# Performance work log

Hardware: AMD Instinct MI355X
Metric: run time of the kernel (lower is better)

## Reference

```python
import jax, jax.numpy as jnp
import numpy as np

N, T, D, H = 32, 4096, 256, 512  # n_mlps, tokens per mlp, d_model, hidden


def setup_inputs() -> dict:
    key = jax.random.key(0)
    k_x, k_w1, k_w2 = jax.random.split(key, 3)
    x = jax.random.normal(k_x, (N, T, D), dtype=jnp.float32)
    # per-MLP weights stacked along the expert dim; init ~ torch Linear default scale
    W1 = jax.random.normal(k_w1, (N, H, D), dtype=jnp.float32) / np.sqrt(D)
    b1 = jnp.zeros((N, H), dtype=jnp.float32)
    W2 = jax.random.normal(k_w2, (N, D, H), dtype=jnp.float32) / np.sqrt(H)
    b2 = jnp.zeros((N, D), dtype=jnp.float32)
    return {"x": x, "W1": W1, "b1": b1, "W2": W2, "b2": b2}


def reference(x, W1, b1, W2, b2):
    # outputs[i] = mlp_i(x[i]); stack + residual add.
    # Expressed as a single grouped (batched) GEMM over the expert dim n.
    h = jnp.einsum('ntd,nhd->nth', x, W1) + b1[:, None, :]   # [N,T,H]
    h = jax.nn.silu(h)
    out = jnp.einsum('nth,ndh->ntd', h, W2) + b2[:, None, :]  # [N,T,D]
    return out + x
```

## Files before the change

### kernel.cpp

```cpp
#include <hip/hip_runtime.h>
#include <hip/hip_bf16.h>


#define N_EXP 32
#define T_TOK 4096
#define D_MOD 256
#define H_HID 512

#define BT 64
#define HC 32
#define NCHUNK 16
#define NTHREADS 256

#define NWELEM 4194304ull
#define WS_NEEDED (8ull * NWELEM)

typedef __attribute__((ext_vector_type(8))) __bf16 bf16x8;
typedef __attribute__((ext_vector_type(4))) __bf16 bf16x4;
typedef __attribute__((ext_vector_type(4))) float  f32x4;
union U4 { uint4 q; bf16x8 v; };

static __device__ __forceinline__ f32x4 mfma16(bf16x8 a, bf16x8 b, f32x4 c) {
  return __builtin_amdgcn_mfma_f32_16x16x32_bf16(a, b, c, 0, 0, 0);
}

static __device__ __forceinline__ void split8(const float v[8], bf16x8& hi, bf16x8& lo) {
#pragma unroll
  for (int j = 0; j < 8; ++j) {
    float f = v[j];
    __bf16 h = (__bf16)f;
    hi[j] = h;
    lo[j] = (__bf16)(f - (float)h);
  }
}

static __device__ __forceinline__ void gl_lds16(const __bf16* g, __bf16* l) {
  __builtin_amdgcn_global_load_lds(
      (const __attribute__((address_space(1))) void*)g,
      (__attribute__((address_space(3))) void*)l, 16, 0, 0);
}

#define BAR_LGKM() do { asm volatile("s_waitcnt lgkmcnt(0)" ::: "memory"); \
  __builtin_amdgcn_s_barrier(); __builtin_amdgcn_sched_barrier(0); } while (0)
#define BAR_VM(n) do { asm volatile("s_waitcnt vmcnt(" #n ")" ::: "memory"); \
  __builtin_amdgcn_s_barrier(); __builtin_amdgcn_sched_barrier(0); } while (0)

__global__ __launch_bounds__(256)
void presplit_w(const float* __restrict__ W1, const float* __restrict__ W2,
                __bf16* __restrict__ ws) {
  unsigned U = blockIdx.x * 256 + threadIdx.x;
  {
    unsigned row = U >> 5;
    unsigned u   = U & 31;
    const float* src = W1 + ((size_t)U << 3);
    float4 a0 = *(const float4*)src, a1 = *(const float4*)(src + 4);
    float v[8] = {a0.x, a0.y, a0.z, a0.w, a1.x, a1.y, a1.z, a1.w};
    bf16x8 hi, lo; split8(v, hi, lo);
    size_t dst = (((size_t)row << 5) | (u ^ (row & 7))) << 3;
    *(bf16x8*)(ws + dst)          = hi;
    *(bf16x8*)(ws + NWELEM + dst) = lo;
  }
  {
    unsigned r = U >> 6;
    unsigned e = r >> 8, d = r & 255;
    unsigned u = U & 63;
    unsigned c = u >> 2, uc = u & 3;
    const float* src = W2 + ((size_t)U << 3);
    float4 a0 = *(const float4*)src, a1 = *(const float4*)(src + 4);
    float v[8] = {a0.x, a0.y, a0.z, a0.w, a1.x, a1.y, a1.z, a1.w};
    bf16x8 hi, lo; split8(v, hi, lo);
    size_t dst = (((((size_t)((e << 4) + c) << 8) + d) << 2) | (uc ^ ((d >> 1) & 3))) << 3;
    *(bf16x8*)(ws + 2 * NWELEM + dst) = hi;
    *(bf16x8*)(ws + 3 * NWELEM + dst) = lo;
  }
}

__global__ __launch_bounds__(NTHREADS, 2)
void pmlp_fused(const float* __restrict__ x, const float* __restrict__ b1g,
                const float* __restrict__ b2g, float* __restrict__ out,
                const __bf16* __restrict__ wsp) {
  __shared__ __bf16 W1h[HC * D_MOD],   W1l[HC * D_MOD];
  __shared__ __bf16 W2h[D_MOD * HC],   W2l[D_MOD * HC];
  __shared__ unsigned APK[BT * 32];
  __shared__ float b1s[H_HID];

  const int tid = threadIdx.x;

  const int p    = blockIdx.x;
  const int xcd  = p & 7;
  const int slot = p >> 3;
  const int e    = xcd + ((slot >> 6) << 3);
  const int ti   = slot & 63;

  const float* xb = x + ((size_t)e * T_TOK + (size_t)ti * BT) * D_MOD;
  float*       ob = out + ((size_t)e * T_TOK + (size_t)ti * BT) * D_MOD;

  const int l    = tid & 63;
  const int w    = tid >> 6;
  const int lrow = l & 15;
  const int lk8  = (l >> 4) << 3;
  const int lr4  = (l >> 4) << 2;
  const int g1_r = w << 4;

  b1s[tid]       = b1g[e * H_HID + tid];
  b1s[tid + 256] = b1g[e * H_HID + tid + 256];

  bf16x8 xh[8], xl[8];
#pragma unroll
  for (int kk = 0; kk < 8; ++kk) {
    const float* s = xb + (g1_r + lrow) * D_MOD + (kk << 5) + lk8;
    float4 u0 = *(const float4*)s;
    float4 u1 = *(const float4*)(s + 4);
    float v[8] = {u0.x, u0.y, u0.z, u0.w, u1.x, u1.y, u1.z, u1.w};
    split8(v, xh[kk], xl[kk]);
  }

  const __bf16* w1h_img = wsp;
  const __bf16* w1l_img = wsp + NWELEM;
  const __bf16* w2h_img = wsp + 2 * NWELEM;
  const __bf16* w2l_img = wsp + 3 * NWELEM;

  auto stageW1 = [&](int c) {
    size_t gb = ((size_t)(e * NCHUNK + c)) << 13;
#pragma unroll
    for (int s = 0; s < 4; ++s) {
      int off = ((w << 2) + s) << 9;
      int go  = off + (l << 3);
      gl_lds16(w1h_img + gb + go, &W1h[off]);
      gl_lds16(w1l_img + gb + go, &W1l[off]);
    }
  };
  auto stageW2 = [&](int c) {
    size_t gb = ((size_t)(e * NCHUNK + c)) << 13;
#pragma unroll
    for (int s = 0; s < 4; ++s) {
      int off = ((w << 2) + s) << 9;
      int go  = off + (l << 3);
      gl_lds16(w2h_img + gb + go, &W2h[off]);
      gl_lds16(w2l_img + gb + go, &W2l[off]);
    }
  };

  const f32x4 fz = {0.f, 0.f, 0.f, 0.f};
  f32x4 acc2[4][4];
#pragma unroll
  for (int mf = 0; mf < 4; ++mf)
#pragma unroll
    for (int nf = 0; nf < 4; ++nf) acc2[mf][nf] = fz;

  asm volatile("" ::: "memory");
  stageW1(0);
  stageW2(0);
  asm volatile("s_waitcnt vmcnt(8)\n\ts_waitcnt lgkmcnt(0)" ::: "memory");
  __builtin_amdgcn_s_barrier();
  __builtin_amdgcn_sched_barrier(0);

  for (int c = 0; c < NCHUNK; ++c) {
    f32x4 acc1[2] = {fz, fz};
    __builtin_amdgcn_s_setprio(1);
#pragma unroll
    for (int kk = 0; kk < 8; ++kk) {
#pragma unroll
      for (int cf = 0; cf < 2; ++cf) {
        int r1 = (cf << 4) + lrow;
        int uu = (((kk << 2) + (lk8 >> 3)) ^ (r1 & 7)) << 3;
        bf16x8 bh = *(const bf16x8*)&W1h[(r1 << 8) + uu];
        bf16x8 bl = *(const bf16x8*)&W1l[(r1 << 8) + uu];
        acc1[cf] = mfma16(xh[kk], bh, acc1[cf]);
        acc1[cf] = mfma16(xh[kk], bl, acc1[cf]);
        acc1[cf] = mfma16(xl[kk], bh, acc1[cf]);
      }
    }
    __builtin_amdgcn_s_setprio(0);
#pragma unroll
    for (int cf = 0; cf < 2; ++cf) {
      int acol = (cf << 4) + lrow;
      float b1v = b1s[c * HC + acol];
#pragma unroll
      for (int r = 0; r < 4; ++r) {
        float hv = acc1[cf][r] + b1v;
        hv = hv / (1.f + __expf(-hv));
        __bf16 hh = (__bf16)hv;
        __bf16 hl = (__bf16)(hv - (float)hh);
        unsigned pk = (unsigned)__builtin_bit_cast(unsigned short, hh) |
                      ((unsigned)__builtin_bit_cast(unsigned short, hl) << 16);
        int arow = g1_r + lr4 + r;
        APK[arow * 32 + ((((acol >> 2) ^ (arow & 7)) << 2) | (acol & 3))] = pk;
      }
    }
    BAR_LGKM();

    if (c < NCHUNK - 1) {
      stageW1(c + 1);
      BAR_VM(8);
    } else {
      BAR_VM(0);
    }

    bf16x8 bh2[4], bl2[4];
#pragma unroll
    for (int nf = 0; nf < 4; ++nf) {
      int dcol = (w << 6) + (nf << 4) + lrow;
      int up = (((lk8 >> 3) ^ ((dcol >> 1) & 3)) << 3);
      bh2[nf] = *(const bf16x8*)&W2h[(dcol << 5) + up];
      bl2[nf] = *(const bf16x8*)&W2l[(dcol << 5) + up];
    }
#pragma unroll
    for (int mf = 0; mf < 4; ++mf) {
      int m  = (mf << 4) + lrow;
      int u1 = lk8 >> 2;
      uint4 qa = *(const uint4*)&APK[m * 32 + ((u1 ^ (m & 7)) << 2)];
      uint4 qb = *(const uint4*)&APK[m * 32 + (((u1 + 1) ^ (m & 7)) << 2)];
      U4 ah, al;
      ah.q.x = (qa.x & 0xFFFFu) | (qa.y << 16);
      ah.q.y = (qa.z & 0xFFFFu) | (qa.w << 16);
      ah.q.z = (qb.x & 0xFFFFu) | (qb.y << 16);
      ah.q.w = (qb.z & 0xFFFFu) | (qb.w << 16);
      al.q.x = (qa.x >> 16) | (qa.y & 0xFFFF0000u);
      al.q.y = (qa.z >> 16) | (qa.w & 0xFFFF0000u);
      al.q.z = (qb.x >> 16) | (qb.y & 0xFFFF0000u);
      al.q.w = (qb.z >> 16) | (qb.w & 0xFFFF0000u);
      __builtin_amdgcn_s_setprio(1);
#pragma unroll
      for (int nf = 0; nf < 4; ++nf) {
        acc2[mf][nf] = mfma16(ah.v, bh2[nf], acc2[mf][nf]);
        acc2[mf][nf] = mfma16(ah.v, bl2[nf], acc2[mf][nf]);
        acc2[mf][nf] = mfma16(al.v, bh2[nf], acc2[mf][nf]);
      }
      __builtin_amdgcn_s_setprio(0);
    }
    BAR_LGKM();

    if (c < NCHUNK - 1) {
      stageW2(c + 1);
      BAR_VM(8);
    }
  }

#pragma unroll
  for (int mf = 0; mf < 4; ++mf)
#pragma unroll
    for (int r = 0; r < 4; ++r) {
      int trow = (mf << 4) + lr4 + r;
#pragma unroll
      for (int nf = 0; nf < 4; ++nf) {
        int dcol = (w << 6) + (nf << 4) + lrow;
        ob[trow * D_MOD + dcol] = acc2[mf][nf][r] + b2g[e * D_MOD + dcol]
                                + xb[trow * D_MOD + dcol];
      }
    }
}

#define WPITCH 264
__global__ __launch_bounds__(NTHREADS, 2)
void pmlp_fb(const float* __restrict__ x, const float* __restrict__ W1,
             const float* __restrict__ b1, const float* __restrict__ W2,
             const float* __restrict__ b2, float* __restrict__ out) {
  __shared__ __bf16 W1h[HC * WPITCH], W1l[HC * WPITCH];
  __shared__ __bf16 W2h[D_MOD * 32],  W2l[D_MOD * 32];
  __shared__ unsigned APK[BT * 32];

  const int tid = threadIdx.x;
  const int p = blockIdx.x, xcd = p & 7, slot = p >> 3;
  const int e = xcd + ((slot >> 6) << 3), ti = slot & 63;
  const float* xb = x + ((size_t)e * T_TOK + (size_t)ti * BT) * D_MOD;
  float*       ob = out + ((size_t)e * T_TOK + (size_t)ti * BT) * D_MOD;
  const int l = tid & 63, w = tid >> 6;
  const int lrow = l & 15, lk8 = (l >> 4) << 3, lr4 = (l >> 4) << 2;
  const int g1_r = w << 4;

  bf16x8 xh[8], xl[8];
#pragma unroll
  for (int kk = 0; kk < 8; ++kk) {
    const float* s = xb + (g1_r + lrow) * D_MOD + (kk << 5) + lk8;
    float4 u0 = *(const float4*)s, u1 = *(const float4*)(s + 4);
    float v[8] = {u0.x, u0.y, u0.z, u0.w, u1.x, u1.y, u1.z, u1.w};
    split8(v, xh[kk], xl[kk]);
  }

  float s1[4][8], s2[4][8];
  auto loadW = [&](int c) {
#pragma unroll
    for (int k2 = 0; k2 < 4; ++k2) {
      int g = tid + (k2 << 8);
      int r1 = g >> 5, c1 = (g & 31) << 3;
      int r2 = g >> 2, c2 = (g & 3) << 3;
      const float* sp1 = W1 + ((size_t)e * H_HID + c * HC + r1) * D_MOD + c1;
      const float* sp2 = W2 + ((size_t)e * D_MOD + r2) * H_HID + c * HC + c2;
      float4 u0 = *(const float4*)sp1, u1 = *(const float4*)(sp1 + 4);
      s1[k2][0]=u0.x; s1[k2][1]=u0.y; s1[k2][2]=u0.z; s1[k2][3]=u0.w;
      s1[k2][4]=u1.x; s1[k2][5]=u1.y; s1[k2][6]=u1.z; s1[k2][7]=u1.w;
      float4 v0 = *(const float4*)sp2, v1 = *(const float4*)(sp2 + 4);
      s2[k2][0]=v0.x; s2[k2][1]=v0.y; s2[k2][2]=v0.z; s2[k2][3]=v0.w;
      s2[k2][4]=v1.x; s2[k2][5]=v1.y; s2[k2][6]=v1.z; s2[k2][7]=v1.w;
    }
  };
  auto writeW = [&]() {
#pragma unroll
    for (int k2 = 0; k2 < 4; ++k2) {
      int g = tid + (k2 << 8);
      int r1 = g >> 5, c1 = (g & 31) << 3;
      int r2 = g >> 2, u2 = g & 3;
      int sw2 = ((u2 ^ (r2 & 3)) << 3);
      bf16x8 hi, lo;
      split8(s1[k2], hi, lo);
      *(bf16x8*)&W1h[r1 * WPITCH + c1] = hi;
      *(bf16x8*)&W1l[r1 * WPITCH + c1] = lo;
      split8(s2[k2], hi, lo);
      *(bf16x8*)&W2h[r2 * 32 + sw2] = hi;
      *(bf16x8*)&W2l[r2 * 32 + sw2] = lo;
    }
  };

  const f32x4 fz = {0.f, 0.f, 0.f, 0.f};
  f32x4 acc2[4][4];
#pragma unroll
  for (int mf = 0; mf < 4; ++mf)
#pragma unroll
    for (int nf = 0; nf < 4; ++nf) acc2[mf][nf] = fz;

  loadW(0); writeW();
  __syncthreads();

  for (int c = 0; c < NCHUNK; ++c) {
    if (c < NCHUNK - 1) loadW(c + 1);
    f32x4 acc1[2] = {fz, fz};
#pragma unroll
    for (int kk = 0; kk < 8; ++kk) {
#pragma unroll
      for (int cf = 0; cf < 2; ++cf) {
        int r1 = (cf << 4) + lrow;
        int k = (kk << 5) + lk8;
        bf16x8 bh = *(const bf16x8*)&W1h[r1 * WPITCH + k];
        bf16x8 bl = *(const bf16x8*)&W1l[r1 * WPITCH + k];
        acc1[cf] = mfma16(xh[kk], bh, acc1[cf]);
        acc1[cf] = mfma16(xh[kk], bl, acc1[cf]);
        acc1[cf] = mfma16(xl[kk], bh, acc1[cf]);
      }
    }
#pragma unroll
    for (int cf = 0; cf < 2; ++cf) {
      int acol = (cf << 4) + lrow;
      float b1v = b1[e * H_HID + c * HC + acol];
#pragma unroll
      for (int r = 0; r < 4; ++r) {
        float hv = acc1[cf][r] + b1v;
        hv = hv / (1.f + __expf(-hv));
        __bf16 hh = (__bf16)hv;
        __bf16 hl = (__bf16)(hv - (float)hh);
        unsigned pk = (unsigned)__builtin_bit_cast(unsigned short, hh) |
                      ((unsigned)__builtin_bit_cast(unsigned short, hl) << 16);
        int arow = g1_r + lr4 + r;
        APK[arow * 32 + ((((acol >> 2) ^ (arow & 7)) << 2) | (acol & 3))] = pk;
      }
    }
    __syncthreads();

    bf16x8 bh2[4], bl2[4];
#pragma unroll
    for (int nf = 0; nf < 4; ++nf) {
      int dcol = (w << 6) + (nf << 4) + lrow;
      int sw = (((lk8 >> 3) ^ (dcol & 3)) << 3);
      bh2[nf] = *(const bf16x8*)&W2h[dcol * 32 + sw];
      bl2[nf] = *(const bf16x8*)&W2l[dcol * 32 + sw];
    }
#pragma unroll
    for (int mf = 0; mf < 4; ++mf) {
      int m = (mf << 4) + lrow, u1 = lk8 >> 2;
      uint4 qa = *(const uint4*)&APK[m * 32 + ((u1 ^ (m & 7)) << 2)];
      uint4 qb = *(const uint4*)&APK[m * 32 + (((u1 + 1) ^ (m & 7)) << 2)];
      U4 ah, al;
      ah.q.x = (qa.x & 0xFFFFu) | (qa.y << 16);
      ah.q.y = (qa.z & 0xFFFFu) | (qa.w << 16);
      ah.q.z = (qb.x & 0xFFFFu) | (qb.y << 16);
      ah.q.w = (qb.z & 0xFFFFu) | (qb.w << 16);
      al.q.x = (qa.x >> 16) | (qa.y & 0xFFFF0000u);
      al.q.y = (qa.z >> 16) | (qa.w & 0xFFFF0000u);
      al.q.z = (qb.x >> 16) | (qb.y & 0xFFFF0000u);
      al.q.w = (qb.z >> 16) | (qb.w & 0xFFFF0000u);
#pragma unroll
      for (int nf = 0; nf < 4; ++nf) {
        acc2[mf][nf] = mfma16(ah.v, bh2[nf], acc2[mf][nf]);
        acc2[mf][nf] = mfma16(ah.v, bl2[nf], acc2[mf][nf]);
        acc2[mf][nf] = mfma16(al.v, bh2[nf], acc2[mf][nf]);
      }
    }
    __syncthreads();
    if (c < NCHUNK - 1) { writeW(); __syncthreads(); }
  }

#pragma unroll
  for (int mf = 0; mf < 4; ++mf)
#pragma unroll
    for (int r = 0; r < 4; ++r) {
      int trow = (mf << 4) + lr4 + r;
#pragma unroll
      for (int nf = 0; nf < 4; ++nf) {
        int dcol = (w << 6) + (nf << 4) + lrow;
        ob[trow * D_MOD + dcol] = acc2[mf][nf][r] + b2[e * D_MOD + dcol]
                                + xb[trow * D_MOD + dcol];
      }
    }
}

extern "C" void kernel_launch(void* const* d_in, const int* in_sizes, int n_in,
                              void* d_out, int out_size, void* d_ws, size_t ws_size,
                              hipStream_t stream) {
  const float* x  = (const float*)d_in[0];
  const float* W1 = (const float*)d_in[1];
  const float* b1 = (const float*)d_in[2];
  const float* W2 = (const float*)d_in[3];
  const float* b2 = (const float*)d_in[4];
  float* out = (float*)d_out;
  __bf16* ws = (__bf16*)d_ws;

  dim3 grid(N_EXP * (T_TOK / BT));
  dim3 block(NTHREADS);

  if (ws_size >= WS_NEEDED) {
    hipLaunchKernelGGL(presplit_w, dim3(2048), dim3(256), 0, stream, W1, W2, ws);
    hipLaunchKernelGGL(pmlp_fused, grid, block, 0, stream,
                       x, b1, b2, out, (const __bf16*)ws);
  } else {
    hipLaunchKernelGGL(pmlp_fb, grid, block, 0, stream, x, W1, b1, W2, b2, out);
  }
}
```

Before: 439.7 us.

## Load W2 fragments directly to registers and split activation LDS into hi/lo arrays

Re-lays out the presplit W2 image in MFMA fragment order so each wave loads its W2 B-operands straight from global memory into registers, dropping the W2 LDS staging and one barrier per chunk. The packed hi/lo activation buffer becomes two separate swizzled bf16 arrays, which removes the unpack bit-twiddling, and the first GEMM splits its accumulators into even and odd chains to shorten MFMA dependency chains. This frees LDS and cuts synchronisation, but the W2 register prefetch raises register pressure and relies on global-load latency being hidden behind the next chunk's first GEMM.

```diff
diff --git a/kernel.cpp b/kernel.cpp
--- a/kernel.cpp
+++ b/kernel.cpp
@@ -18,7 +18,6 @@
 typedef __attribute__((ext_vector_type(8))) __bf16 bf16x8;
 typedef __attribute__((ext_vector_type(4))) __bf16 bf16x4;
 typedef __attribute__((ext_vector_type(4))) float  f32x4;
-union U4 { uint4 q; bf16x8 v; };
 
 static __device__ __forceinline__ f32x4 mfma16(bf16x8 a, bf16x8 b, f32x4 c) {
   return __builtin_amdgcn_mfma_f32_16x16x32_bf16(a, b, c, 0, 0, 0);
@@ -42,7 +41,8 @@
 
 #define BAR_LGKM() do { asm volatile("s_waitcnt lgkmcnt(0)" ::: "memory"); \
   __builtin_amdgcn_s_barrier(); __builtin_amdgcn_sched_barrier(0); } while (0)
-#define BAR_VM(n) do { asm volatile("s_waitcnt vmcnt(" #n ")" ::: "memory"); \
+#define BAR_VM_LGKM(n) do { \
+  asm volatile("s_waitcnt vmcnt(" #n ") lgkmcnt(0)" ::: "memory"); \
   __builtin_amdgcn_s_barrier(); __builtin_amdgcn_sched_barrier(0); } while (0)
 
 __global__ __launch_bounds__(256)
@@ -61,17 +61,19 @@
     *(bf16x8*)(ws + NWELEM + dst) = lo;
   }
   {
-    unsigned r = U >> 6;
-    unsigned e = r >> 8, d = r & 255;
-    unsigned u = U & 63;
-    unsigned c = u >> 2, uc = u & 3;
+    unsigned uh = U & 63;
+    unsigned r  = U >> 6;
+    unsigned e  = r >> 8, d = r & 255;
+    unsigned c  = uh >> 2, kg = uh & 3;
+    unsigned w  = d >> 6, nf = (d >> 4) & 3;
+    unsigned lane = kg * 16 + (d & 15);
     const float* src = W2 + ((size_t)U << 3);
     float4 a0 = *(const float4*)src, a1 = *(const float4*)(src + 4);
     float v[8] = {a0.x, a0.y, a0.z, a0.w, a1.x, a1.y, a1.z, a1.w};
     bf16x8 hi, lo; split8(v, hi, lo);
-    size_t dst = (((((size_t)((e << 4) + c) << 8) + d) << 2) | (uc ^ ((d >> 1) & 3))) << 3;
-    *(bf16x8*)(ws + 2 * NWELEM + dst) = hi;
-    *(bf16x8*)(ws + 3 * NWELEM + dst) = lo;
+    size_t V = ((((size_t)(e * 16 + c) * 4 + w) * 4 + nf) * 64 + lane) << 3;
+    *(bf16x8*)(ws + 2 * NWELEM + V) = hi;
+    *(bf16x8*)(ws + 3 * NWELEM + V) = lo;
   }
 }
 
@@ -79,10 +81,9 @@
 void pmlp_fused(const float* __restrict__ x, const float* __restrict__ b1g,
                 const float* __restrict__ b2g, float* __restrict__ out,
                 const __bf16* __restrict__ wsp) {
-  __shared__ __bf16 W1h[HC * D_MOD],   W1l[HC * D_MOD];
-  __shared__ __bf16 W2h[D_MOD * HC],   W2l[D_MOD * HC];
-  __shared__ unsigned APK[BT * 32];
-  __shared__ float b1s[H_HID];
+  __shared__ __bf16 W1h[HC * D_MOD], W1l[HC * D_MOD];
+  __shared__ __bf16 Ah[BT * HC],     Al[BT * HC];
+  __shared__ float  b1s[H_HID];
 
   const int tid = threadIdx.x;
 
@@ -129,15 +130,17 @@
       gl_lds16(w1h_img + gb + go, &W1h[off]);
       gl_lds16(w1l_img + gb + go, &W1l[off]);
     }
+    __builtin_amdgcn_sched_barrier(0);
   };
-  auto stageW2 = [&](int c) {
-    size_t gb = ((size_t)(e * NCHUNK + c)) << 13;
-#pragma unroll
-    for (int s = 0; s < 4; ++s) {
-      int off = ((w << 2) + s) << 9;
-      int go  = off + (l << 3);
-      gl_lds16(w2h_img + gb + go, &W2h[off]);
-      gl_lds16(w2l_img + gb + go, &W2l[off]);
+
+  bf16x8 bh2[4], bl2[4];
+  auto loadW2 = [&](int c) {
+    size_t base = (((size_t)(e * NCHUNK + c) * 4 + w) * 4) << 9;
+#pragma unroll
+    for (int nf = 0; nf < 4; ++nf) {
+      size_t o = base + (((size_t)nf << 6) + l) * 8;
+      bh2[nf] = *(const bf16x8*)(w2h_img + o);
+      bl2[nf] = *(const bf16x8*)(w2l_img + o);
     }
   };
 
@@ -150,13 +153,13 @@
 
   asm volatile("" ::: "memory");
   stageW1(0);
-  stageW2(0);
-  asm volatile("s_waitcnt vmcnt(8)\n\ts_waitcnt lgkmcnt(0)" ::: "memory");
+  loadW2(0);
+  asm volatile("s_waitcnt vmcnt(8) lgkmcnt(0)" ::: "memory");
   __builtin_amdgcn_s_barrier();
   __builtin_amdgcn_sched_barrier(0);
 
   for (int c = 0; c < NCHUNK; ++c) {
-    f32x4 acc1[2] = {fz, fz};
+    f32x4 a1e[2] = {fz, fz}, a1o[2] = {fz, fz};
     __builtin_amdgcn_s_setprio(1);
 #pragma unroll
     for (int kk = 0; kk < 8; ++kk) {
@@ -166,74 +169,54 @@
         int uu = (((kk << 2) + (lk8 >> 3)) ^ (r1 & 7)) << 3;
         bf16x8 bh = *(const bf16x8*)&W1h[(r1 << 8) + uu];
         bf16x8 bl = *(const bf16x8*)&W1l[(r1 << 8) + uu];
-        acc1[cf] = mfma16(xh[kk], bh, acc1[cf]);
-        acc1[cf] = mfma16(xh[kk], bl, acc1[cf]);
-        acc1[cf] = mfma16(xl[kk], bh, acc1[cf]);
+        f32x4* acc = (kk & 1) ? &a1o[cf] : &a1e[cf];
+        *acc = mfma16(xh[kk], bh, *acc);
+        *acc = mfma16(xh[kk], bl, *acc);
+        *acc = mfma16(xl[kk], bh, *acc);
       }
     }
     __builtin_amdgcn_s_setprio(0);
+
 #pragma unroll
     for (int cf = 0; cf < 2; ++cf) {
       int acol = (cf << 4) + lrow;
       float b1v = b1s[c * HC + acol];
+      f32x4 hsum = a1e[cf] + a1o[cf];
 #pragma unroll
       for (int r = 0; r < 4; ++r) {
-        float hv = acc1[cf][r] + b1v;
+        float hv = hsum[r] + b1v;
         hv = hv / (1.f + __expf(-hv));
         __bf16 hh = (__bf16)hv;
         __bf16 hl = (__bf16)(hv - (float)hh);
-        unsigned pk = (unsigned)__builtin_bit_cast(unsigned short, hh) |
-                      ((unsigned)__builtin_bit_cast(unsigned short, hl) << 16);
         int arow = g1_r + lr4 + r;
-        APK[arow * 32 + ((((acol >> 2) ^ (arow & 7)) << 2) | (acol & 3))] = pk;
+        int idx = (arow << 5) + (((acol >> 3) ^ ((arow >> 1) & 3)) << 3) + (acol & 7);
+        Ah[idx] = hh;
+        Al[idx] = hl;
       }
     }
     BAR_LGKM();
 
-    if (c < NCHUNK - 1) {
-      stageW1(c + 1);
-      BAR_VM(8);
-    } else {
-      BAR_VM(0);
-    }
-
-    bf16x8 bh2[4], bl2[4];
-#pragma unroll
-    for (int nf = 0; nf < 4; ++nf) {
-      int dcol = (w << 6) + (nf << 4) + lrow;
-      int up = (((lk8 >> 3) ^ ((dcol >> 1) & 3)) << 3);
-      bh2[nf] = *(const bf16x8*)&W2h[(dcol << 5) + up];
-      bl2[nf] = *(const bf16x8*)&W2l[(dcol << 5) + up];
-    }
+    if (c < NCHUNK - 1) stageW1(c + 1);
+
 #pragma unroll
     for (int mf = 0; mf < 4; ++mf) {
       int m  = (mf << 4) + lrow;
-      int u1 = lk8 >> 2;
-      uint4 qa = *(const uint4*)&APK[m * 32 + ((u1 ^ (m & 7)) << 2)];
-      uint4 qb = *(const uint4*)&APK[m * 32 + (((u1 + 1) ^ (m & 7)) << 2)];
-      U4 ah, al;
-      ah.q.x = (qa.x & 0xFFFFu) | (qa.y << 16);
-      ah.q.y = (qa.z & 0xFFFFu) | (qa.w << 16);
-      ah.q.z = (qb.x & 0xFFFFu) | (qb.y << 16);
-      ah.q.w = (qb.z & 0xFFFFu) | (qb.w << 16);
-      al.q.x = (qa.x >> 16) | (qa.y & 0xFFFF0000u);
-      al.q.y = (qa.z >> 16) | (qa.w & 0xFFFF0000u);
-      al.q.z = (qb.x >> 16) | (qb.y & 0xFFFF0000u);
-      al.q.w = (qb.z >> 16) | (qb.w & 0xFFFF0000u);
+      int su = ((lk8 >> 3) ^ ((m >> 1) & 3)) << 3;
+      bf16x8 ah = *(const bf16x8*)&Ah[(m << 5) + su];
+      bf16x8 al = *(const bf16x8*)&Al[(m << 5) + su];
       __builtin_amdgcn_s_setprio(1);
 #pragma unroll
       for (int nf = 0; nf < 4; ++nf) {
-        acc2[mf][nf] = mfma16(ah.v, bh2[nf], acc2[mf][nf]);
-        acc2[mf][nf] = mfma16(ah.v, bl2[nf], acc2[mf][nf]);
-        acc2[mf][nf] = mfma16(al.v, bh2[nf], acc2[mf][nf]);
+        acc2[mf][nf] = mfma16(ah, bh2[nf], acc2[mf][nf]);
+        acc2[mf][nf] = mfma16(ah, bl2[nf], acc2[mf][nf]);
+        acc2[mf][nf] = mfma16(al, bh2[nf], acc2[mf][nf]);
       }
       __builtin_amdgcn_s_setprio(0);
     }
-    BAR_LGKM();
 
     if (c < NCHUNK - 1) {
-      stageW2(c + 1);
-      BAR_VM(8);
+      loadW2(c + 1);
+      BAR_VM_LGKM(8);
     }
   }
 
@@ -252,6 +235,7 @@
 }
 
 #define WPITCH 264
+union U4 { uint4 q; bf16x8 v; };
 __global__ __launch_bounds__(NTHREADS, 2)
 void pmlp_fb(const float* __restrict__ x, const float* __restrict__ W1,
              const float* __restrict__ b1, const float* __restrict__ W2,
```

Result: no change. 433.8 us (-1.3%).
